# Optimization experiments

Hardware: AMD Instinct MI355X
Metric: run time of the kernel (lower is better)

## Reference

```python
import jax, jax.numpy as jnp
import numpy as np

B, D_IN, D_H = 8192, 512, 1024


def setup_inputs() -> dict:
    key = jax.random.key(0)
    ks = jax.random.split(key, 5)
    # Kaiming-normal-ish init: std = sqrt(2/fan_in)
    Wx = jax.random.normal(ks[0], (D_IN, 4 * D_H), jnp.float32) * np.sqrt(2.0 / D_IN)
    Wh = jax.random.normal(ks[1], (D_H, 4 * D_H), jnp.float32) * np.sqrt(2.0 / D_H)
    b = jnp.zeros((4 * D_H,), jnp.float32)
    x = jax.random.normal(ks[2], (B, D_IN), jnp.float32)
    h = jax.random.normal(ks[3], (B, D_H), jnp.float32)
    c = jax.random.normal(ks[4], (B, D_H), jnp.float32)
    return {"x": x, "h": h, "c": c, "Wx": Wx, "Wh": Wh, "b": b}


def reference(x, h, c, Wx, Wh, b):
    # Fused gate pre-activations: [B, 4H] in gate order (g, i, f, o)
    gates = x @ Wx + h @ Wh + b[None, :]
    g_in, i_in, f_in, o_in = jnp.split(gates, 4, axis=-1)
    g_out = jnp.tanh(g_in)
    i_out = jax.nn.sigmoid(i_in)
    # NOTE: faithful to the original source's bug — f_out and o_out both use i_in.
    f_out = jax.nn.sigmoid(i_in)
    o_out = jax.nn.sigmoid(i_in)
    c_new = g_out * i_out + f_out * c
    h_new = jnp.tanh(c_new) * o_out
    return h_new, c_new
```

## Files before the change

### kernel.cpp

```cpp
#include <hip/hip_runtime.h>
#include <hip/hip_bf16.h>
#include <cstdint>

#define BROWS 8192
#define DIN   512
#define DH    1024
#define KTOT  1536
#define NT    (KTOT / 64)

typedef __bf16 bf16x8 __attribute__((ext_vector_type(8)));
typedef __bf16 bf16x4 __attribute__((ext_vector_type(4)));
typedef float  f32x4  __attribute__((ext_vector_type(4)));

__device__ __forceinline__ void load16_to_lds(const void* gptr, void* lptr) {
    __builtin_amdgcn_global_load_lds(
        (const __attribute__((address_space(1))) uint32_t*)gptr,
        (__attribute__((address_space(3))) uint32_t*)lptr,
        16, 0, 0);
}

__global__ __launch_bounds__(256) void cvtA_kernel(
    const float* __restrict__ x, const float* __restrict__ h,
    __bf16* __restrict__ A) {
    int t = blockIdx.x * 256 + threadIdx.x;
    int row = t / 192;
    int j = t - row * 192;
    int kg = j * 8;
    const float* src = (kg < DIN) ? (x + (size_t)row * DIN + kg)
                                  : (h + (size_t)row * DH + (kg - DIN));
    float4 u = *(const float4*)src;
    float4 v = *(const float4*)(src + 4);
    bf16x8 o = { (__bf16)u.x, (__bf16)u.y, (__bf16)u.z, (__bf16)u.w,
                 (__bf16)v.x, (__bf16)v.y, (__bf16)v.z, (__bf16)v.w };
    int swz = (j * 16) ^ ((row & 7) << 4);
    *(bf16x8*)((char*)A + (size_t)row * 3072 + swz) = o;
}

__global__ __launch_bounds__(256) void cvtB_kernel(
    const float* __restrict__ Wx, const float* __restrict__ Wh,
    __bf16* __restrict__ Bt) {
    __shared__ float tile[32][33];
    int k0 = blockIdx.x * 32;
    int n0 = blockIdx.y * 32;
    int tx = threadIdx.x;
    int ty = threadIdx.y;
#pragma unroll
    for (int i = 0; i < 4; ++i) {
        int k = k0 + ty + 8 * i;
        float v = (k < DIN) ? Wx[(size_t)k * 4096 + n0 + tx]
                            : Wh[(size_t)(k - DIN) * 4096 + n0 + tx];
        tile[ty + 8 * i][tx] = v;
    }
    __syncthreads();
    int n = n0 + tx;
    int kk = ty * 4;
    bf16x4 o = { (__bf16)tile[kk][tx], (__bf16)tile[kk + 1][tx],
                 (__bf16)tile[kk + 2][tx], (__bf16)tile[kk + 3][tx] };
    int swz = ((k0 + kk) * 2) ^ ((n & 7) << 4);
    *(bf16x4*)((char*)Bt + (size_t)n * 3072 + swz) = o;
}


#define BARRIER  do { __builtin_amdgcn_sched_barrier(0); __builtin_amdgcn_s_barrier(); __builtin_amdgcn_sched_barrier(0); } while (0)
#define VMW(n)   do { asm volatile("s_waitcnt vmcnt(" #n ")" ::: "memory"); __builtin_amdgcn_sched_barrier(0); } while (0)
#define LGKM0    do { asm volatile("s_waitcnt lgkmcnt(0)" ::: "memory"); __builtin_amdgcn_sched_barrier(0); } while (0)

#define STAGE(obuf, kt) do {                                                   \
    _Pragma("unroll")                                                          \
    for (int p_ = 0; p_ < 4; ++p_) {                                           \
        int row_ = p_ * 64 + r0;                                               \
        load16_to_lds(Ab + (size_t)(brow + row_) * 3072 + (kt) * 128 + cb,     \
                      sAb + (obuf) + row_ * 128 + cb);                         \
    }                                                                          \
    load16_to_lds(Bb + (size_t)(bnp + r0) * 3072 + (kt) * 128 + cb,            \
                  sAb + (obuf) + 32768 + r0 * 128 + cb);                       \
    load16_to_lds(Bb + (size_t)(1024 + bnp + r0) * 3072 + (kt) * 128 + cb,     \
                  sAb + (obuf) + 32768 + (64 + r0) * 128 + cb);                \
    __builtin_amdgcn_sched_barrier(0);                                         \
} while (0)

#define READS(obuf) do {                                                       \
    _Pragma("unroll")                                                          \
    for (int m_ = 0; m_ < 4; ++m_) {                                           \
        _Pragma("unroll")                                                      \
        for (int ks_ = 0; ks_ < 2; ++ks_) {                                    \
            aF[m_][ks_] = *(const bf16x8*)(sAb + (obuf)                        \
                + (wrow + m_ * 16 + l15) * 128                                 \
                + ((ks_ * 64 + l4x16) ^ swzkey));                              \
        }                                                                      \
    }                                                                          \
    _Pragma("unroll")                                                          \
    for (int n_ = 0; n_ < 2; ++n_) {                                           \
        _Pragma("unroll")                                                      \
        for (int ks_ = 0; ks_ < 2; ++ks_) {                                    \
            bgF[n_][ks_] = *(const bf16x8*)(sAb + (obuf) + 32768               \
                + (wcol + n_ * 16 + l15) * 128                                 \
                + ((ks_ * 64 + l4x16) ^ swzkey));                              \
            biF[n_][ks_] = *(const bf16x8*)(sAb + (obuf) + 32768               \
                + (64 + wcol + n_ * 16 + l15) * 128                            \
                + ((ks_ * 64 + l4x16) ^ swzkey));                              \
        }                                                                      \
    }                                                                          \
} while (0)

#define MMA_ALL() do {                                                         \
    __builtin_amdgcn_s_setprio(1);                                             \
    _Pragma("unroll")                                                          \
    for (int ks_ = 0; ks_ < 2; ++ks_) {                                        \
        _Pragma("unroll")                                                      \
        for (int m_ = 0; m_ < 4; ++m_) {                                       \
            _Pragma("unroll")                                                  \
            for (int n_ = 0; n_ < 2; ++n_) {                                   \
                accg[m_][n_] = __builtin_amdgcn_mfma_f32_16x16x32_bf16(        \
                    aF[m_][ks_], bgF[n_][ks_], accg[m_][n_], 0, 0, 0);         \
                acci[m_][n_] = __builtin_amdgcn_mfma_f32_16x16x32_bf16(        \
                    aF[m_][ks_], biF[n_][ks_], acci[m_][n_], 0, 0, 0);         \
            }                                                                  \
        }                                                                      \
    }                                                                          \
    __builtin_amdgcn_s_setprio(0);                                             \
    __builtin_amdgcn_sched_barrier(0);                                         \
} while (0)

__global__ __launch_bounds__(512) void lstm_gemm_kernel(
    const __bf16* __restrict__ A,
    const __bf16* __restrict__ Bt,
    const float* __restrict__ bias,
    const float* __restrict__ c_in,
    float* __restrict__ out_h,
    float* __restrict__ out_c) {
    __shared__ char smem[147456];

    const int tid  = threadIdx.x;
    const int lane = tid & 63;
    const int wid  = tid >> 6;
    const int wr   = wid & 3;
    const int wc   = wid >> 2;

    const int bid   = blockIdx.x;
    const int band  = (bid & 7) * 4 + ((bid >> 3) & 3);
    const int panel = bid >> 5;
    const int brow  = band * 256;
    const int bnp   = panel * 64;

    const int l15    = lane & 15;
    const int l4x16  = (lane >> 4) * 16;
    const int swzkey = (l15 & 7) << 4;
    const int wrow   = wr * 64;
    const int wcol   = wc * 32;

    const int r0 = tid >> 3;
    const int cb = (tid & 7) * 16;

    const char* Ab = (const char*)A;
    const char* Bb = (const char*)Bt;
    char* sAb = smem;

    f32x4 accg[4][2], acci[4][2];
#pragma unroll
    for (int mi = 0; mi < 4; ++mi)
#pragma unroll
        for (int ni = 0; ni < 2; ++ni) {
            accg[mi][ni] = (f32x4){0.f, 0.f, 0.f, 0.f};
            acci[mi][ni] = (f32x4){0.f, 0.f, 0.f, 0.f};
        }

    bf16x8 aF[4][2], bgF[2][2], biF[2][2];

    STAGE(0, 0);
    STAGE(49152, 1);

    int o0 = 0, o1 = 49152, o2 = 98304;
    for (int t = 0; t < NT - 2; ++t) {
        STAGE(o2, t + 2);
        VMW(12);
        BARRIER;
        READS(o0);
        LGKM0;
        BARRIER;
        MMA_ALL();
        int tmp = o0; o0 = o1; o1 = o2; o2 = tmp;
    }
    {
        VMW(6); BARRIER;
        READS(o0);
        LGKM0; BARRIER;
        MMA_ALL();
        int tmp = o0; o0 = o1; o1 = o2; o2 = tmp;
    }
    {
        VMW(0); BARRIER;
        READS(o0);
        LGKM0;
        MMA_ALL();
    }

    const int R0 = brow + wrow;
    const int C0 = bnp + wcol;
    const int l4 = lane >> 4;
#pragma unroll
    for (int ni = 0; ni < 2; ++ni) {
        const int col = C0 + ni * 16 + l15;
        const float bg = bias[col];
        const float bi = bias[1024 + col];
#pragma unroll
        for (int mi = 0; mi < 4; ++mi) {
#pragma unroll
            for (int r = 0; r < 4; ++r) {
                const int row = R0 + mi * 16 + l4 * 4 + r;
                const float g_in = accg[mi][ni][r] + bg;
                const float i_in = acci[mi][ni][r] + bi;
                const float s  = 1.0f / (1.0f + __expf(-i_in));
                const float tg = 2.0f / (1.0f + __expf(-2.0f * g_in)) - 1.0f;
                const float cv = c_in[(size_t)row * DH + col];
                const float cn = s * (tg + cv);
                const float hn = (2.0f / (1.0f + __expf(-2.0f * cn)) - 1.0f) * s;
                out_h[(size_t)row * DH + col] = hn;
                out_c[(size_t)row * DH + col] = cn;
            }
        }
    }
}

extern "C" void kernel_launch(void* const* d_in, const int* in_sizes, int n_in,
                              void* d_out, int out_size, void* d_ws, size_t ws_size,
                              hipStream_t stream) {
    const float* x  = (const float*)d_in[0];
    const float* h  = (const float*)d_in[1];
    const float* c  = (const float*)d_in[2];
    const float* Wx = (const float*)d_in[3];
    const float* Wh = (const float*)d_in[4];
    const float* b  = (const float*)d_in[5];

    __bf16* A  = (__bf16*)d_ws;
    __bf16* Bt = (__bf16*)((char*)d_ws + (size_t)BROWS * KTOT * 2);

    float* out_h = (float*)d_out;
    float* out_c = out_h + (size_t)BROWS * DH;

    cvtA_kernel<<<(BROWS * (KTOT / 8)) / 256, 256, 0, stream>>>(x, h, A);
    cvtB_kernel<<<dim3(KTOT / 32, 2048 / 32), dim3(32, 8), 0, stream>>>(Wx, Wh, Bt);
    lstm_gemm_kernel<<<512, 512, 0, stream>>>(A, Bt, b, c, out_h, out_c);
}
```

Measured before the change: 86.21 us.

## Widen GEMM tile to 256x128 per gate and double-buffer LDS with split-k register prefetch

Each block now computes 128 output columns per gate instead of 64, which halves the grid to 256 blocks and doubles A-tile reuse from LDS. The LDS pipeline moves from a triple buffer with a full read-then-compute step to a double buffer. LDS fragment reads for the second k-half are interleaved with MFMAs on the first, with partial lgkmcnt waits. Accumulator register use doubles (128 floats per thread), which raises register pressure. With 256 blocks on a 256-CU part there is exactly one wave of blocks, and global prefetch depth drops to one tile ahead.

```diff
diff --git a/kernel.cpp b/kernel.cpp
--- a/kernel.cpp
+++ b/kernel.cpp
@@ -63,59 +63,53 @@
 
 #define BARRIER  do { __builtin_amdgcn_sched_barrier(0); __builtin_amdgcn_s_barrier(); __builtin_amdgcn_sched_barrier(0); } while (0)
 #define VMW(n)   do { asm volatile("s_waitcnt vmcnt(" #n ")" ::: "memory"); __builtin_amdgcn_sched_barrier(0); } while (0)
-#define LGKM0    do { asm volatile("s_waitcnt lgkmcnt(0)" ::: "memory"); __builtin_amdgcn_sched_barrier(0); } while (0)
-
-#define STAGE(obuf, kt) do {                                                   \
+#define LGKM(n)  do { asm volatile("s_waitcnt lgkmcnt(" #n ")" ::: "memory"); __builtin_amdgcn_sched_barrier(0); } while (0)
+
+#define STAGE(cur, kt) do {                                                    \
     _Pragma("unroll")                                                          \
     for (int p_ = 0; p_ < 4; ++p_) {                                           \
         int row_ = p_ * 64 + r0;                                               \
         load16_to_lds(Ab + (size_t)(brow + row_) * 3072 + (kt) * 128 + cb,     \
-                      sAb + (obuf) + row_ * 128 + cb);                         \
-    }                                                                          \
-    load16_to_lds(Bb + (size_t)(bnp + r0) * 3072 + (kt) * 128 + cb,            \
-                  sAb + (obuf) + 32768 + r0 * 128 + cb);                       \
-    load16_to_lds(Bb + (size_t)(1024 + bnp + r0) * 3072 + (kt) * 128 + cb,     \
-                  sAb + (obuf) + 32768 + (64 + r0) * 128 + cb);                \
+                      smem + (cur) * 65536 + row_ * 128 + cb);                 \
+    }                                                                          \
+    _Pragma("unroll")                                                          \
+    for (int p_ = 0; p_ < 2; ++p_) {                                           \
+        int row_ = p_ * 64 + r0;                                               \
+        load16_to_lds(Bb + (size_t)(bnp + row_) * 3072 + (kt) * 128 + cb,      \
+                      smem + (cur) * 65536 + 32768 + row_ * 128 + cb);         \
+        load16_to_lds(Bb + (size_t)(1024 + bnp + row_) * 3072                  \
+                          + (kt) * 128 + cb,                                   \
+                      smem + (cur) * 65536 + 32768 + (128 + row_) * 128 + cb); \
+    }                                                                          \
     __builtin_amdgcn_sched_barrier(0);                                         \
 } while (0)
 
-#define READS(obuf) do {                                                       \
+#define READF(ks, cur, aT, bgT, biT) do {                                      \
+    const int kb_ = (((ks) * 64 + l4x16) ^ swzkey);                            \
+    _Pragma("unroll")                                                          \
+    for (int m_ = 0; m_ < 4; ++m_)                                             \
+        aT[m_] = *(const bf16x8*)(smem + (cur) * 65536                         \
+            + (wrow + m_ * 16 + l15) * 128 + kb_);                             \
+    _Pragma("unroll")                                                          \
+    for (int n_ = 0; n_ < 4; ++n_) {                                           \
+        bgT[n_] = *(const bf16x8*)(smem + (cur) * 65536 + 32768                \
+            + (wcol + n_ * 16 + l15) * 128 + kb_);                             \
+        biT[n_] = *(const bf16x8*)(smem + (cur) * 65536 + 32768                \
+            + (128 + wcol + n_ * 16 + l15) * 128 + kb_);                       \
+    }                                                                          \
+    __builtin_amdgcn_sched_barrier(0);                                         \
+} while (0)
+
+#define MMA(aT, bgT, biT) do {                                                 \
+    __builtin_amdgcn_s_setprio(1);                                             \
     _Pragma("unroll")                                                          \
     for (int m_ = 0; m_ < 4; ++m_) {                                           \
         _Pragma("unroll")                                                      \
-        for (int ks_ = 0; ks_ < 2; ++ks_) {                                    \
-            aF[m_][ks_] = *(const bf16x8*)(sAb + (obuf)                        \
-                + (wrow + m_ * 16 + l15) * 128                                 \
-                + ((ks_ * 64 + l4x16) ^ swzkey));                              \
-        }                                                                      \
-    }                                                                          \
-    _Pragma("unroll")                                                          \
-    for (int n_ = 0; n_ < 2; ++n_) {                                           \
-        _Pragma("unroll")                                                      \
-        for (int ks_ = 0; ks_ < 2; ++ks_) {                                    \
-            bgF[n_][ks_] = *(const bf16x8*)(sAb + (obuf) + 32768               \
-                + (wcol + n_ * 16 + l15) * 128                                 \
-                + ((ks_ * 64 + l4x16) ^ swzkey));                              \
-            biF[n_][ks_] = *(const bf16x8*)(sAb + (obuf) + 32768               \
-                + (64 + wcol + n_ * 16 + l15) * 128                            \
-                + ((ks_ * 64 + l4x16) ^ swzkey));                              \
-        }                                                                      \
-    }                                                                          \
-} while (0)
-
-#define MMA_ALL() do {                                                         \
-    __builtin_amdgcn_s_setprio(1);                                             \
-    _Pragma("unroll")                                                          \
-    for (int ks_ = 0; ks_ < 2; ++ks_) {                                        \
-        _Pragma("unroll")                                                      \
-        for (int m_ = 0; m_ < 4; ++m_) {                                       \
-            _Pragma("unroll")                                                  \
-            for (int n_ = 0; n_ < 2; ++n_) {                                   \
-                accg[m_][n_] = __builtin_amdgcn_mfma_f32_16x16x32_bf16(        \
-                    aF[m_][ks_], bgF[n_][ks_], accg[m_][n_], 0, 0, 0);         \
-                acci[m_][n_] = __builtin_amdgcn_mfma_f32_16x16x32_bf16(        \
-                    aF[m_][ks_], biF[n_][ks_], acci[m_][n_], 0, 0, 0);         \
-            }                                                                  \
+        for (int n_ = 0; n_ < 4; ++n_) {                                       \
+            accg[m_][n_] = __builtin_amdgcn_mfma_f32_16x16x32_bf16(            \
+                aT[m_], bgT[n_], accg[m_][n_], 0, 0, 0);                       \
+            acci[m_][n_] = __builtin_amdgcn_mfma_f32_16x16x32_bf16(            \
+                aT[m_], biT[n_], acci[m_][n_], 0, 0, 0);                       \
         }                                                                      \
     }                                                                          \
     __builtin_amdgcn_s_setprio(0);                                             \
@@ -129,7 +123,7 @@
     const float* __restrict__ c_in,
     float* __restrict__ out_h,
     float* __restrict__ out_c) {
-    __shared__ char smem[147456];
+    __shared__ char smem[131072];
 
     const int tid  = threadIdx.x;
     const int lane = tid & 63;
@@ -141,65 +135,61 @@
     const int band  = (bid & 7) * 4 + ((bid >> 3) & 3);
     const int panel = bid >> 5;
     const int brow  = band * 256;
-    const int bnp   = panel * 64;
+    const int bnp   = panel * 128;
 
     const int l15    = lane & 15;
     const int l4x16  = (lane >> 4) * 16;
     const int swzkey = (l15 & 7) << 4;
     const int wrow   = wr * 64;
-    const int wcol   = wc * 32;
+    const int wcol   = wc * 64;
 
     const int r0 = tid >> 3;
     const int cb = (tid & 7) * 16;
 
     const char* Ab = (const char*)A;
     const char* Bb = (const char*)Bt;
-    char* sAb = smem;
-
-    f32x4 accg[4][2], acci[4][2];
+
+    f32x4 accg[4][4], acci[4][4];
 #pragma unroll
     for (int mi = 0; mi < 4; ++mi)
 #pragma unroll
-        for (int ni = 0; ni < 2; ++ni) {
+        for (int ni = 0; ni < 4; ++ni) {
             accg[mi][ni] = (f32x4){0.f, 0.f, 0.f, 0.f};
             acci[mi][ni] = (f32x4){0.f, 0.f, 0.f, 0.f};
         }
 
-    bf16x8 aF[4][2], bgF[2][2], biF[2][2];
+    bf16x8 aX[4], bgX[4], biX[4];
+    bf16x8 aY[4], bgY[4], biY[4];
 
     STAGE(0, 0);
-    STAGE(49152, 1);
-
-    int o0 = 0, o1 = 49152, o2 = 98304;
-    for (int t = 0; t < NT - 2; ++t) {
-        STAGE(o2, t + 2);
-        VMW(12);
+    STAGE(1, 1);
+    VMW(8);
+    BARRIER;
+    READF(0, 0, aX, bgX, biX);
+
+    for (int t = 0; t < NT; ++t) {
+        const int cur = t & 1;
+        READF(1, cur, aY, bgY, biY);
+        LGKM(12);
+        MMA(aX, bgX, biX);
+        LGKM(0);
         BARRIER;
-        READS(o0);
-        LGKM0;
-        BARRIER;
-        MMA_ALL();
-        int tmp = o0; o0 = o1; o1 = o2; o2 = tmp;
-    }
-    {
-        VMW(6); BARRIER;
-        READS(o0);
-        LGKM0; BARRIER;
-        MMA_ALL();
-        int tmp = o0; o0 = o1; o1 = o2; o2 = tmp;
-    }
-    {
-        VMW(0); BARRIER;
-        READS(o0);
-        LGKM0;
-        MMA_ALL();
+        if (t + 2 < NT) {
+            STAGE(cur, t + 2);
+        }
+        if (t + 1 < NT) {
+            if (t + 2 < NT) { VMW(8); } else { VMW(0); }
+            BARRIER;
+            READF(0, cur ^ 1, aX, bgX, biX);
+        }
+        MMA(aY, bgY, biY);
     }
 
     const int R0 = brow + wrow;
     const int C0 = bnp + wcol;
     const int l4 = lane >> 4;
 #pragma unroll
-    for (int ni = 0; ni < 2; ++ni) {
+    for (int ni = 0; ni < 4; ++ni) {
         const int col = C0 + ni * 16 + l15;
         const float bg = bias[col];
         const float bi = bias[1024 + col];
@@ -240,5 +230,5 @@
 
     cvtA_kernel<<<(BROWS * (KTOT / 8)) / 256, 256, 0, stream>>>(x, h, A);
     cvtB_kernel<<<dim3(KTOT / 32, 2048 / 32), dim3(32, 8), 0, stream>>>(Wx, Wh, Bt);
-    lstm_gemm_kernel<<<512, 512, 0, stream>>>(A, Bt, b, c, out_h, out_c);
-}
+    lstm_gemm_kernel<<<256, 512, 0, stream>>>(A, Bt, b, c, out_h, out_c);
+}
```

Result: faster. 82.12 us (-4.7%).
